# Kernel optimization log

Hardware: AMD Instinct MI355X
Metric: run time of the kernel (lower is better)

## Reference

```python
import jax, jax.numpy as jnp
import numpy as np

TEMPERATURE = 1.0  # module default current_temperature
TOP_K = 2
NUM_EXPERTS = 64
EPS = 1e-10


def setup_inputs() -> dict:
    key = jax.random.key(0)
    k1, k2 = jax.random.split(key)
    x = jax.random.normal(k1, (4, 4096, 2048), dtype=jnp.float32)
    # nn.Linear(d_model, num_experts) weight has shape [num_experts, d_model]
    W_gate = jax.random.normal(k2, (NUM_EXPERTS, 2048), dtype=jnp.float32) * (1.0 / np.sqrt(2048))
    return {"x": x, "W_gate": W_gate}


def reference(x, W_gate):
    # Gate GEMM: [B,S,D] x [E,D] -> [B,S,E]
    logits = jnp.einsum("bsd,ed->bse", x, W_gate)
    scaled = logits / TEMPERATURE
    # Full distribution over experts (for load-balancing loss)
    router_probs = jax.nn.softmax(scaled, axis=-1)
    # Top-k selection over the expert dim, then renormalize via softmax
    top_k_logits, top_k_indices = jax.lax.top_k(scaled, TOP_K)  # [B,S,K]
    top_k_weights = jax.nn.softmax(top_k_logits, axis=-1)
    # Routing stats (no-grad in torch; plain values here)
    entropy = -jnp.sum(router_probs * jnp.log(router_probs + EPS), axis=-1)
    routing_entropy = entropy.mean()
    selection_confidence = top_k_weights[:, :, 0].mean()
    counts = jnp.zeros((NUM_EXPERTS,), dtype=x.dtype).at[top_k_indices.reshape(-1)].add(1.0)
    expert_utilization = counts / (counts.sum() + EPS)
    return (top_k_weights, top_k_indices, router_probs,
            routing_entropy, selection_confidence, expert_utilization)
```

## Files before the change

kernel.cpp:

```cpp
#include <hip/hip_runtime.h>
#include <math.h>

#define NTOK 16384
#define DIM 2048
#define NEXP 64
#define KS 8
#define CPG 8
#define TPB 512
#define NTB 32

#define OFF_W    0
#define OFF_I    32768
#define OFF_P    65536
#define OFF_ENT  1114112
#define OFF_CONF 1114113
#define OFF_UTIL 1114114

#define PLG_OFF  196608
#define PLG_STRIDE 1048576
#define WS_NEED_STRIDED (786432ull + 33554432ull)

typedef short s16x8 __attribute__((ext_vector_type(8)));
typedef float f32x4 __attribute__((ext_vector_type(4)));

__device__ __forceinline__ unsigned short f2bf(float v) {
    unsigned u = __builtin_bit_cast(unsigned, v);
    u = u + 0x7FFFu + ((u >> 16) & 1u);
    return (unsigned short)(u >> 16);
}
__device__ __forceinline__ float bf2f(unsigned short b) {
    return __builtin_bit_cast(float, (unsigned)b << 16);
}

__global__ void router_wsplit(const float* __restrict__ Wg, uint4* __restrict__ wsp,
                              float* __restrict__ out) {
    const int bid = blockIdx.x;
    const int tid = threadIdx.x;
    const int c   = bid >> 2;
    const int gt  = (bid & 3) * 64 + tid;
    if (c == 0 && gt < 66) out[OFF_ENT + gt] = 0.0f;
    const int nt = gt >> 6, l = gt & 63;
    const int e  = 16 * nt + (l & 15);
    const int k0 = 32 * c + 8 * (l >> 4);
    const float* src = Wg + (size_t)e * DIM + k0;
    float4 a = *(const float4*)src;
    float4 b = *(const float4*)(src + 4);
    float v[8] = {a.x, a.y, a.z, a.w, b.x, b.y, b.z, b.w};
    unsigned short H[8], M[8], L[8];
    #pragma unroll
    for (int j = 0; j < 8; ++j) {
        H[j] = f2bf(v[j]);  float r = v[j] - bf2f(H[j]);
        M[j] = f2bf(r);     r = r - bf2f(M[j]);
        L[j] = f2bf(r);
    }
    uint4 ph, pm, pl;
    ph.x = H[0] | ((unsigned)H[1] << 16); ph.y = H[2] | ((unsigned)H[3] << 16);
    ph.z = H[4] | ((unsigned)H[5] << 16); ph.w = H[6] | ((unsigned)H[7] << 16);
    pm.x = M[0] | ((unsigned)M[1] << 16); pm.y = M[2] | ((unsigned)M[3] << 16);
    pm.z = M[4] | ((unsigned)M[5] << 16); pm.w = M[6] | ((unsigned)M[7] << 16);
    pl.x = L[0] | ((unsigned)L[1] << 16); pl.y = L[2] | ((unsigned)L[3] << 16);
    pl.z = L[4] | ((unsigned)L[5] << 16); pl.w = L[6] | ((unsigned)L[7] << 16);
    const int idx = c * 256 + gt;
    wsp[idx]         = ph;
    wsp[16384 + idx] = pm;
    wsp[32768 + idx] = pl;
}

__global__ void router_zero(float* __restrict__ p) {
    ((float4*)p)[blockIdx.x * 256 + threadIdx.x] = make_float4(0.f, 0.f, 0.f, 0.f);
}

#define CONVA3(a0_, a1_, AH_, AM_, AL_) {                                \
    float xv[8];                                                         \
    xv[0]=a0_.x; xv[1]=a0_.y; xv[2]=a0_.z; xv[3]=a0_.w;                  \
    xv[4]=a1_.x; xv[5]=a1_.y; xv[6]=a1_.z; xv[7]=a1_.w;                  \
    _Pragma("unroll")                                                    \
    for (int j = 0; j < 8; ++j) {                                        \
        unsigned u_  = __builtin_bit_cast(unsigned, xv[j]);              \
        unsigned hb_ = u_ & 0xFFFF0000u;                                 \
        float    r_  = xv[j] - __builtin_bit_cast(float, hb_);           \
        unsigned mb_ = __builtin_bit_cast(unsigned, r_) & 0xFFFF0000u;   \
        float    r2_ = r_ - __builtin_bit_cast(float, mb_);              \
        unsigned lb_ = __builtin_bit_cast(unsigned, r2_);                \
        AH_[j] = (short)(hb_ >> 16);                                     \
        AM_[j] = (short)(mb_ >> 16);                                     \
        AL_[j] = (short)(lb_ >> 16);                                     \
    } }

#define MF(A_, B_, C_) __builtin_amdgcn_mfma_f32_16x16x32_bf16(A_, B_, C_, 0, 0, 0)
#define BC(q_) __builtin_bit_cast(s16x8, q_)

#define PR8(A0_, A1_, Bq_) {                                             \
    s16x8 b0_ = BC(Bq_[0]), b1_ = BC(Bq_[1]);                            \
    s16x8 b2_ = BC(Bq_[2]), b3_ = BC(Bq_[3]);                            \
    a00 = MF(A0_, b0_, a00); a01 = MF(A0_, b1_, a01);                    \
    a02 = MF(A0_, b2_, a02); a03 = MF(A0_, b3_, a03);                    \
    a10 = MF(A1_, b0_, a10); a11 = MF(A1_, b1_, a11);                    \
    a12 = MF(A1_, b2_, a12); a13 = MF(A1_, b3_, a13); }

template<bool STRIDED>
__global__ __launch_bounds__(1024, 4) void router_main(
    const float* __restrict__ x, const uint4* __restrict__ wq,
    float* __restrict__ pl)
{
    extern __shared__ uint4 Wl[];

    const int tid = threadIdx.x;
    const int l   = tid & 63;
    const int w   = tid >> 6;
    const int tr  = l & 15;
    const int qd  = l >> 4;
    const int kg  = blockIdx.x >> 5;
    const int tb  = blockIdx.x & 31;
    const int tw0 = tb * TPB + w * 32;

    #pragma unroll
    for (int j = 0; j < 6; ++j) {
        int flat = j * 1024 + tid;
        int p = flat >> 11, rem = flat & 2047;
        int c = rem >> 8,  q  = rem & 255;
        Wl[flat] = wq[p * 16384 + (kg * CPG + c) * 256 + q];
    }
    __syncthreads();

    const float* xb0 = x + (size_t)(tw0 + tr) * DIM + kg * (CPG * 32) + 8 * qd;
    const float* xb1 = xb0 + 16 * DIM;

    f32x4 a00 = (f32x4)(0.f), a01 = (f32x4)(0.f), a02 = (f32x4)(0.f), a03 = (f32x4)(0.f);
    f32x4 a10 = (f32x4)(0.f), a11 = (f32x4)(0.f), a12 = (f32x4)(0.f), a13 = (f32x4)(0.f);
    s16x8 ah0, am0, al0, ah1, am1, al1;
    uint4 bhq[4], bmq[4], blq[4];
    float4 Xc0, Xc1, Xc2, Xc3, Xn0, Xn1, Xn2, Xn3;

    Xc0 = *(const float4*)(xb0);      Xc1 = *(const float4*)(xb0 + 4);
    Xc2 = *(const float4*)(xb1);      Xc3 = *(const float4*)(xb1 + 4);

    #pragma unroll
    for (int c = 0; c < CPG; ++c) {
        if (c + 1 < CPG) {
            Xn0 = *(const float4*)(xb0 + (c + 1) * 32);
            Xn1 = *(const float4*)(xb0 + (c + 1) * 32 + 4);
            Xn2 = *(const float4*)(xb1 + (c + 1) * 32);
            Xn3 = *(const float4*)(xb1 + (c + 1) * 32 + 4);
        }
        #pragma unroll
        for (int nt = 0; nt < 4; ++nt) {
            bhq[nt] = Wl[(0 * CPG + c) * 256 + nt * 64 + l];
            bmq[nt] = Wl[(1 * CPG + c) * 256 + nt * 64 + l];
            blq[nt] = Wl[(2 * CPG + c) * 256 + nt * 64 + l];
        }
        CONVA3(Xc0, Xc1, ah0, am0, al0);
        CONVA3(Xc2, Xc3, ah1, am1, al1);
        PR8(ah0, ah1, bhq);
        PR8(am0, am1, bhq);
        PR8(ah0, ah1, bmq);
        PR8(am0, am1, bmq);
        PR8(ah0, ah1, blq);
        PR8(al0, al1, bhq);
        if (c + 1 < CPG) { Xc0 = Xn0; Xc1 = Xn1; Xc2 = Xn2; Xc3 = Xn3; }
    }

    float* dst = STRIDED ? (pl + (size_t)kg * PLG_STRIDE) : pl;
#define STACC(acc_, tt_, nt_) { _Pragma("unroll")                        \
    for (int r = 0; r < 4; ++r) {                                        \
        int tok = tw0 + (tt_) * 16 + 4 * qd + r;                         \
        int ex_ = (nt_) * 16 + tr;                                       \
        if constexpr (STRIDED) dst[(size_t)tok * 64 + ex_] = acc_[r];    \
        else atomicAdd(&dst[(size_t)tok * 64 + ex_], acc_[r]);           \
    } }
    STACC(a00, 0, 0); STACC(a01, 0, 1); STACC(a02, 0, 2); STACC(a03, 0, 3);
    STACC(a10, 1, 0); STACC(a11, 1, 1); STACC(a12, 1, 2); STACC(a13, 1, 3);
#undef STACC
}

__device__ __forceinline__ void merge2(float& m1, int& i1, float& m2, int& i2,
                                       float om1, int oi1, float om2, int oi2) {
    bool of = (om1 > m1) || (om1 == m1 && oi1 < i1);
    float n1, n2; int j1, j2;
    if (of) {
        n1 = om1; j1 = oi1;
        bool s = (m1 > om2) || (m1 == om2 && i1 < oi2);
        n2 = s ? m1 : om2; j2 = s ? i1 : oi2;
    } else {
        n1 = m1; j1 = i1;
        bool s = (om1 > m2) || (om1 == m2 && oi1 < i2);
        n2 = s ? om1 : m2; j2 = s ? oi1 : i2;
    }
    m1 = n1; i1 = j1; m2 = n2; i2 = j2;
}

template<int NPART>
__global__ void router_post(const float* __restrict__ plg, float* __restrict__ out) {
    __shared__ float s_ent, s_conf, s_cnt[NEXP];
    const int tid  = threadIdx.x;
    const int lane = tid & 63;
    const int wv   = tid >> 6;
    if (tid == 0) { s_ent = 0.f; s_conf = 0.f; }
    if (tid < NEXP) s_cnt[tid] = 0.f;
    __syncthreads();

    const int tb = blockIdx.x * 32 + wv * 8;
    float entA = 0.f, confA = 0.f;

    for (int k = 0; k < 8; ++k) {
        const int t = tb + k;
        float lgv = 0.f;
        #pragma unroll
        for (int p = 0; p < NPART; ++p)
            lgv += plg[(size_t)p * PLG_STRIDE + (size_t)t * 64 + lane];

        float m1 = lgv, m2 = -INFINITY;
        int   i1 = lane, i2 = 127;
        #pragma unroll
        for (int off = 32; off >= 1; off >>= 1) {
            float om1 = __shfl_xor(m1, off);
            int   oi1 = __shfl_xor(i1, off);
            float om2 = __shfl_xor(m2, off);
            int   oi2 = __shfl_xor(i2, off);
            merge2(m1, i1, m2, i2, om1, oi1, om2, oi2);
        }
        float d  = lgv - m1;
        float ex = __expf(d);
        float ss = ex, ts = d * ex;
        #pragma unroll
        for (int off = 32; off >= 1; off >>= 1) {
            ss += __shfl_xor(ss, off);
            ts += __shfl_xor(ts, off);
        }
        float rs = 1.0f / ss;
        out[OFF_P + (size_t)t * 64 + lane] = ex * rs;
        if (lane == 0) {
            float H  = logf(ss) - ts * rs;
            float e2 = __expf(m2 - m1);
            float rn = 1.0f / (1.0f + e2);
            *(float2*)&out[OFF_W + 2 * t] = make_float2(rn, e2 * rn);
            *(float2*)&out[OFF_I + 2 * t] = make_float2((float)i1, (float)i2);
            entA  += H;
            confA += rn;
            atomicAdd(&s_cnt[i1], 1.0f);
            atomicAdd(&s_cnt[i2], 1.0f);
        }
    }
    if (lane == 0) { atomicAdd(&s_ent, entA); atomicAdd(&s_conf, confA); }
    __syncthreads();
    if (tid == 0) {
        atomicAdd(&out[OFF_ENT],  s_ent  * (1.0f / 16384.0f));
        atomicAdd(&out[OFF_CONF], s_conf * (1.0f / 16384.0f));
    }
    if (tid < NEXP)
        atomicAdd(&out[OFF_UTIL + tid], s_cnt[tid] * (1.0f / 32768.0f));
}

extern "C" void kernel_launch(void* const* d_in, const int* in_sizes, int n_in,
                              void* d_out, int out_size, void* d_ws, size_t ws_size,
                              hipStream_t stream) {
    const float* x  = (const float*)d_in[0];
    const float* Wg = (const float*)d_in[1];
    float* out = (float*)d_out;
    float* plg = (float*)d_ws + PLG_OFF;
    (void)in_sizes; (void)n_in; (void)out_size;

    router_wsplit<<<dim3(256), dim3(64), 0, stream>>>(Wg, (uint4*)d_ws, out);
    if (ws_size >= WS_NEED_STRIDED) {
        router_main<true><<<dim3(NTB * KS), dim3(1024), 98304, stream>>>(
            x, (const uint4*)d_ws, plg);
        router_post<KS><<<dim3(512), dim3(256), 0, stream>>>(plg, out);
    } else {
        router_zero<<<dim3(1024), dim3(256), 0, stream>>>(plg);
        router_main<false><<<dim3(NTB * KS), dim3(1024), 98304, stream>>>(
            x, (const uint4*)d_ws, plg);
        router_post<1><<<dim3(512), dim3(256), 0, stream>>>(plg, out);
    }
}
```

Before: 245.0 us.

## Stream x through per-wave LDS ring via global_load_lds with register-held weights

Restructures the gate GEMM main kernel. Blocks drop from 1024 threads to 256 and each covers 128 tokens over a quarter of the K dimension, so the K split falls from 8 to 4 and the partial-logit workspace halves. x tiles are streamed into a swizzled 4-deep per-wave LDS ring with async global_load_lds, synchronised by manual vmcnt waits. Weight fragments are double-buffered in registers straight from global memory instead of being staged in LDS. The aim is to overlap x loads with MFMA work and cut LDS weight traffic, at the cost of higher register pressure and fragile hand-written wait counts.

```diff
diff --git a/kernel.cpp b/kernel.cpp
--- a/kernel.cpp
+++ b/kernel.cpp
@@ -4,10 +4,10 @@
 #define NTOK 16384
 #define DIM 2048
 #define NEXP 64
-#define KS 8
-#define CPG 8
-#define TPB 512
-#define NTB 32
+#define KG 4
+#define NC 16
+#define WTOK 32
+#define BTOK 128
 
 #define OFF_W    0
 #define OFF_I    32768
@@ -18,7 +18,7 @@
 
 #define PLG_OFF  196608
 #define PLG_STRIDE 1048576
-#define WS_NEED_STRIDED (786432ull + 33554432ull)
+#define WS_NEED_STRIDED (786432ull + 16777216ull)
 
 typedef short s16x8 __attribute__((ext_vector_type(8)));
 typedef float f32x4 __attribute__((ext_vector_type(4)));
@@ -30,6 +30,12 @@
 }
 __device__ __forceinline__ float bf2f(unsigned short b) {
     return __builtin_bit_cast(float, (unsigned)b << 16);
+}
+
+__device__ __forceinline__ void gload16(const void* g, void* l) {
+    __builtin_amdgcn_global_load_lds(
+        (const __attribute__((address_space(1))) unsigned int*)g,
+        (__attribute__((address_space(3))) unsigned int*)l, 16, 0, 0);
 }
 
 __global__ void router_wsplit(const float* __restrict__ Wg, uint4* __restrict__ wsp,
@@ -70,7 +76,7 @@
     ((float4*)p)[blockIdx.x * 256 + threadIdx.x] = make_float4(0.f, 0.f, 0.f, 0.f);
 }
 
-#define CONVA3(a0_, a1_, AH_, AM_, AL_) {                                \
+#define CONVA3(a0_, a1_) {                                               \
     float xv[8];                                                         \
     xv[0]=a0_.x; xv[1]=a0_.y; xv[2]=a0_.z; xv[3]=a0_.w;                  \
     xv[4]=a1_.x; xv[5]=a1_.y; xv[6]=a1_.z; xv[7]=a1_.w;                  \
@@ -82,94 +88,106 @@
         unsigned mb_ = __builtin_bit_cast(unsigned, r_) & 0xFFFF0000u;   \
         float    r2_ = r_ - __builtin_bit_cast(float, mb_);              \
         unsigned lb_ = __builtin_bit_cast(unsigned, r2_);                \
-        AH_[j] = (short)(hb_ >> 16);                                     \
-        AM_[j] = (short)(mb_ >> 16);                                     \
-        AL_[j] = (short)(lb_ >> 16);                                     \
+        ah[j] = (short)(hb_ >> 16);                                      \
+        am[j] = (short)(mb_ >> 16);                                      \
+        al[j] = (short)(lb_ >> 16);                                      \
     } }
 
 #define MF(A_, B_, C_) __builtin_amdgcn_mfma_f32_16x16x32_bf16(A_, B_, C_, 0, 0, 0)
 #define BC(q_) __builtin_bit_cast(s16x8, q_)
 
-#define PR8(A0_, A1_, Bq_) {                                             \
-    s16x8 b0_ = BC(Bq_[0]), b1_ = BC(Bq_[1]);                            \
-    s16x8 b2_ = BC(Bq_[2]), b3_ = BC(Bq_[3]);                            \
-    a00 = MF(A0_, b0_, a00); a01 = MF(A0_, b1_, a01);                    \
-    a02 = MF(A0_, b2_, a02); a03 = MF(A0_, b3_, a03);                    \
-    a10 = MF(A1_, b0_, a10); a11 = MF(A1_, b1_, a11);                    \
-    a12 = MF(A1_, b2_, a12); a13 = MF(A1_, b3_, a13); }
+#define STAGE(c_) { _Pragma("unroll")                                    \
+    for (int i_ = 0; i_ < 4; ++i_) {                                     \
+        const int tau_ = 8 * i_ + (l >> 3);                              \
+        const int gs_  = ((l & 7) >> 1) ^ (tau_ & 3);                    \
+        gload16(xw + (size_t)tau_ * DIM + (c_) * 32 + gs_ * 8 + (l & 1) * 4, \
+                &ring[wv][(c_) & 3][8 * i_][0]);                         \
+    } }
+
+#define READA(tt_, c_) {                                                 \
+    const int tau_ = (tt_) * 16 + tr;                                    \
+    const int sl_  = qd ^ (tau_ & 3);                                    \
+    const uint4* row_ = &ring[wv][(c_) & 3][tau_][0];                    \
+    float4 a0_ = __builtin_bit_cast(float4, row_[2 * sl_]);              \
+    float4 a1_ = __builtin_bit_cast(float4, row_[2 * sl_ + 1]);          \
+    CONVA3(a0_, a1_);                                                    \
+    }
+
+#define LOADW12(W_, c_) { const int b_ = (kg * NC + (c_)) * 256 + l;     \
+    W_[0] = wq[b_];          W_[1] = wq[b_ + 64];                        \
+    W_[2] = wq[b_ + 128];    W_[3] = wq[b_ + 192];                       \
+    W_[4] = wq[16384 + b_];       W_[5] = wq[16384 + b_ + 64];           \
+    W_[6] = wq[16384 + b_ + 128]; W_[7] = wq[16384 + b_ + 192];          \
+    W_[8] = wq[32768 + b_];       W_[9] = wq[32768 + b_ + 64];           \
+    W_[10] = wq[32768 + b_ + 128]; W_[11] = wq[32768 + b_ + 192]; }
+
+#define PR4(F_, W_, o_, Q0_, Q1_, Q2_, Q3_) {                            \
+    Q0_ = MF(F_, BC(W_[(o_) + 0]), Q0_);                                 \
+    Q1_ = MF(F_, BC(W_[(o_) + 1]), Q1_);                                 \
+    Q2_ = MF(F_, BC(W_[(o_) + 2]), Q2_);                                 \
+    Q3_ = MF(F_, BC(W_[(o_) + 3]), Q3_); }
+
+#define COMPUTE24(W_, Q0_, Q1_, Q2_, Q3_) {                              \
+    PR4(ah, W_, 0, Q0_, Q1_, Q2_, Q3_);                                  \
+    PR4(am, W_, 0, Q0_, Q1_, Q2_, Q3_);                                  \
+    PR4(ah, W_, 4, Q0_, Q1_, Q2_, Q3_);                                  \
+    PR4(am, W_, 4, Q0_, Q1_, Q2_, Q3_);                                  \
+    PR4(ah, W_, 8, Q0_, Q1_, Q2_, Q3_);                                  \
+    PR4(al, W_, 0, Q0_, Q1_, Q2_, Q3_); }
+
+#define PHASE(c_, W_) {                                                  \
+    if ((c_) + 3 < NC) STAGE((c_) + 3);                                  \
+    asm volatile("s_waitcnt vmcnt(8)" ::: "memory");                     \
+    __builtin_amdgcn_sched_barrier(0);                                   \
+    READA(0, c_);                                                        \
+    COMPUTE24(W_, q00, q01, q02, q03);                                   \
+    READA(1, c_);                                                        \
+    COMPUTE24(W_, q10, q11, q12, q13);                                   \
+    if ((c_) + 2 < NC) LOADW12(W_, (c_) + 2);                            \
+    }
 
 template<bool STRIDED>
-__global__ __launch_bounds__(1024, 4) void router_main(
+__global__ __launch_bounds__(256, 2) void router_main(
     const float* __restrict__ x, const uint4* __restrict__ wq,
-    float* __restrict__ pl)
+    float* __restrict__ plg)
 {
-    extern __shared__ uint4 Wl[];
+    __shared__ __align__(16) uint4 ring[4][4][WTOK][8];
 
     const int tid = threadIdx.x;
     const int l   = tid & 63;
-    const int w   = tid >> 6;
+    const int wv  = tid >> 6;
     const int tr  = l & 15;
     const int qd  = l >> 4;
-    const int kg  = blockIdx.x >> 5;
-    const int tb  = blockIdx.x & 31;
-    const int tw0 = tb * TPB + w * 32;
+    const int kg  = blockIdx.x & 3;
+    const int bt0 = (blockIdx.x >> 2) * BTOK;
+    const int t0w = bt0 + wv * WTOK;
+
+    const float* xw = x + (size_t)t0w * DIM + kg * (NC * 32);
+
+    f32x4 q00 = (f32x4)(0.f), q01 = (f32x4)(0.f), q02 = (f32x4)(0.f), q03 = (f32x4)(0.f);
+    f32x4 q10 = (f32x4)(0.f), q11 = (f32x4)(0.f), q12 = (f32x4)(0.f), q13 = (f32x4)(0.f);
+    s16x8 ah, am, al;
+    uint4 wA[12], wB[12];
+
+    STAGE(0); STAGE(1); STAGE(2);
+    LOADW12(wA, 0); LOADW12(wB, 1);
 
     #pragma unroll
-    for (int j = 0; j < 6; ++j) {
-        int flat = j * 1024 + tid;
-        int p = flat >> 11, rem = flat & 2047;
-        int c = rem >> 8,  q  = rem & 255;
-        Wl[flat] = wq[p * 16384 + (kg * CPG + c) * 256 + q];
-    }
-    __syncthreads();
-
-    const float* xb0 = x + (size_t)(tw0 + tr) * DIM + kg * (CPG * 32) + 8 * qd;
-    const float* xb1 = xb0 + 16 * DIM;
-
-    f32x4 a00 = (f32x4)(0.f), a01 = (f32x4)(0.f), a02 = (f32x4)(0.f), a03 = (f32x4)(0.f);
-    f32x4 a10 = (f32x4)(0.f), a11 = (f32x4)(0.f), a12 = (f32x4)(0.f), a13 = (f32x4)(0.f);
-    s16x8 ah0, am0, al0, ah1, am1, al1;
-    uint4 bhq[4], bmq[4], blq[4];
-    float4 Xc0, Xc1, Xc2, Xc3, Xn0, Xn1, Xn2, Xn3;
-
-    Xc0 = *(const float4*)(xb0);      Xc1 = *(const float4*)(xb0 + 4);
-    Xc2 = *(const float4*)(xb1);      Xc3 = *(const float4*)(xb1 + 4);
-
-    #pragma unroll
-    for (int c = 0; c < CPG; ++c) {
-        if (c + 1 < CPG) {
-            Xn0 = *(const float4*)(xb0 + (c + 1) * 32);
-            Xn1 = *(const float4*)(xb0 + (c + 1) * 32 + 4);
-            Xn2 = *(const float4*)(xb1 + (c + 1) * 32);
-            Xn3 = *(const float4*)(xb1 + (c + 1) * 32 + 4);
-        }
-        #pragma unroll
-        for (int nt = 0; nt < 4; ++nt) {
-            bhq[nt] = Wl[(0 * CPG + c) * 256 + nt * 64 + l];
-            bmq[nt] = Wl[(1 * CPG + c) * 256 + nt * 64 + l];
-            blq[nt] = Wl[(2 * CPG + c) * 256 + nt * 64 + l];
-        }
-        CONVA3(Xc0, Xc1, ah0, am0, al0);
-        CONVA3(Xc2, Xc3, ah1, am1, al1);
-        PR8(ah0, ah1, bhq);
-        PR8(am0, am1, bhq);
-        PR8(ah0, ah1, bmq);
-        PR8(am0, am1, bmq);
-        PR8(ah0, ah1, blq);
-        PR8(al0, al1, bhq);
-        if (c + 1 < CPG) { Xc0 = Xn0; Xc1 = Xn1; Xc2 = Xn2; Xc3 = Xn3; }
-    }
-
-    float* dst = STRIDED ? (pl + (size_t)kg * PLG_STRIDE) : pl;
+    for (int c = 0; c < NC; c += 2) {
+        PHASE(c, wA);
+        PHASE(c + 1, wB);
+    }
+
+    float* dst = STRIDED ? (plg + (size_t)kg * PLG_STRIDE) : plg;
 #define STACC(acc_, tt_, nt_) { _Pragma("unroll")                        \
     for (int r = 0; r < 4; ++r) {                                        \
-        int tok = tw0 + (tt_) * 16 + 4 * qd + r;                         \
+        int tok = t0w + (tt_) * 16 + 4 * qd + r;                         \
         int ex_ = (nt_) * 16 + tr;                                       \
         if constexpr (STRIDED) dst[(size_t)tok * 64 + ex_] = acc_[r];    \
         else atomicAdd(&dst[(size_t)tok * 64 + ex_], acc_[r]);           \
     } }
-    STACC(a00, 0, 0); STACC(a01, 0, 1); STACC(a02, 0, 2); STACC(a03, 0, 3);
-    STACC(a10, 1, 0); STACC(a11, 1, 1); STACC(a12, 1, 2); STACC(a13, 1, 3);
+    STACC(q00, 0, 0); STACC(q01, 0, 1); STACC(q02, 0, 2); STACC(q03, 0, 3);
+    STACC(q10, 1, 0); STACC(q11, 1, 1); STACC(q12, 1, 2); STACC(q13, 1, 3);
 #undef STACC
 }
 
@@ -262,12 +280,12 @@
 
     router_wsplit<<<dim3(256), dim3(64), 0, stream>>>(Wg, (uint4*)d_ws, out);
     if (ws_size >= WS_NEED_STRIDED) {
-        router_main<true><<<dim3(NTB * KS), dim3(1024), 98304, stream>>>(
+        router_main<true><<<dim3((NTOK / BTOK) * KG), dim3(256), 0, stream>>>(
             x, (const uint4*)d_ws, plg);
-        router_post<KS><<<dim3(512), dim3(256), 0, stream>>>(plg, out);
+        router_post<KG><<<dim3(512), dim3(256), 0, stream>>>(plg, out);
     } else {
         router_zero<<<dim3(1024), dim3(256), 0, stream>>>(plg);
-        router_main<false><<<dim3(NTB * KS), dim3(1024), 98304, stream>>>(
+        router_main<false><<<dim3((NTOK / BTOK) * KG), dim3(256), 0, stream>>>(
             x, (const uint4*)d_ws, plg);
         router_post<1><<<dim3(512), dim3(256), 0, stream>>>(plg, out);
     }
```

New measurement: 240.5 us. About the same (-1.8%).
